# Kernel optimization log

Measured on AMD Instinct MI355X. Metric: run time of the kernel, lower is better.

## Reference

```python
import jax, jax.numpy as jnp
import numpy as np

B, S, D = 4, 2048, 1024
H = 16
HD = D // H  # head_dim = 64

def setup_inputs() -> dict:
    key = jax.random.key(0)
    kx, kq, ko = jax.random.split(key, 3)
    # xavier-uniform-like scale for weights
    lim_qkv = (6.0 / (D + 3 * D)) ** 0.5
    lim_o = (6.0 / (D + D)) ** 0.5
    return {
        "x": jax.random.normal(kx, (B, S, D), dtype=jnp.float32),
        "w_qkv": jax.random.uniform(kq, (3 * D, D), jnp.float32, -lim_qkv, lim_qkv),
        "b_qkv": jnp.zeros((3 * D,), jnp.float32),
        "w_o": jax.random.uniform(ko, (D, D), jnp.float32, -lim_o, lim_o),
        "b_o": jnp.zeros((D,), jnp.float32),
    }

def reference(x, w_qkv, b_qkv, w_o, b_o):
    b, s, _ = x.shape
    # QKV projection: torch Linear computes x @ W^T + b
    qkv = jnp.einsum("bsd,ed->bse", x, w_qkv) + b_qkv          # [B,S,3D]
    qkv = qkv.reshape(b, s, H, 3 * HD).transpose(0, 2, 1, 3)    # [B,H,S,3*hd]
    q, k, v = jnp.split(qkv, 3, axis=-1)                        # each [B,H,S,hd]
    scale = 1.0 / jnp.sqrt(jnp.asarray(HD, dtype=q.dtype))
    logits = jnp.einsum("bhqd,bhkd->bhqk", q, k) * scale        # [B,H,S,S]
    attn = jax.nn.softmax(logits, axis=-1)
    vals = jnp.einsum("bhqk,bhkd->bhqd", attn, v)               # [B,H,S,hd]
    vals = vals.transpose(0, 2, 1, 3).reshape(b, s, H * HD)     # [B,S,D]
    return jnp.einsum("bsd,ed->bse", vals, w_o) + b_o
```

## Files before the change

### kernel.cpp

```cpp
#include <hip/hip_runtime.h>
#include <hip/hip_bf16.h>


typedef __attribute__((ext_vector_type(4))) float f32x4;
typedef __attribute__((ext_vector_type(8))) short s16x8;
typedef __attribute__((ext_vector_type(2))) unsigned u32x2;
typedef __attribute__((ext_vector_type(4))) unsigned u32x4;

constexpr size_t PART_ELEMS = (size_t)8192 * 1024;

__device__ __forceinline__ unsigned short f2bf(float f) {
  __hip_bfloat16 h = __float2bfloat16(f);
  unsigned short u;
  __builtin_memcpy(&u, &h, 2);
  return u;
}
__device__ __forceinline__ unsigned pack2bf(float a, float b) {
  return (unsigned)f2bf(a) | ((unsigned)f2bf(b) << 16);
}
__device__ __forceinline__ float fexp2(float x) {
#if __has_builtin(__builtin_amdgcn_exp2f)
  return __builtin_amdgcn_exp2f(x);
#else
  float r; asm("v_exp_f32 %0, %1" : "=v"(r) : "v"(x)); return r;
#endif
}
__device__ __forceinline__ void gload_lds16(const void* g, void* l) {
  __builtin_amdgcn_global_load_lds(
      (const __attribute__((address_space(1))) unsigned*)g,
      (__attribute__((address_space(3))) unsigned*)l, 16, 0, 0);
}
__device__ __forceinline__ int swzs(int row, int col) {
  return row * 64 + (((col >> 3) ^ (row & 7)) << 3) + (col & 7);
}

__global__ __launch_bounds__(256) void cvt2_kernel(
    const float* __restrict__ a, unsigned short* __restrict__ oa,
    const float* __restrict__ b, unsigned short* __restrict__ ob) {
  const int bid = blockIdx.x;
  const float* in;
  unsigned short* out;
  size_t i;
  if (bid < 4096) {
    in = a; out = oa; i = ((size_t)bid * 256 + threadIdx.x) * 8;
  } else {
    in = b; out = ob; i = ((size_t)(bid - 4096) * 256 + threadIdx.x) * 8;
  }
  f32x4 v0 = *reinterpret_cast<const f32x4*>(in + i);
  f32x4 v1 = *reinterpret_cast<const f32x4*>(in + i + 4);
  u32x4 pk;
  pk.x = pack2bf(v0.x, v0.y); pk.y = pack2bf(v0.z, v0.w);
  pk.z = pack2bf(v1.x, v1.y); pk.w = pack2bf(v1.z, v1.w);
  *reinterpret_cast<u32x4*>(out + i) = pk;
}

__global__ __launch_bounds__(256) void cvt_kernel(const float* __restrict__ in,
                                                  unsigned short* __restrict__ out) {
  const size_t i = ((size_t)blockIdx.x * 256 + threadIdx.x) * 8;
  f32x4 v0 = *reinterpret_cast<const f32x4*>(in + i);
  f32x4 v1 = *reinterpret_cast<const f32x4*>(in + i + 4);
  u32x4 pk;
  pk.x = pack2bf(v0.x, v0.y); pk.y = pack2bf(v0.z, v0.w);
  pk.z = pack2bf(v1.x, v1.y); pk.w = pack2bf(v1.z, v1.w);
  *reinterpret_cast<u32x4*>(out + i) = pk;
}

template <bool SCATTER>
__global__ __launch_bounds__(256) void gemm_bb(
    const unsigned short* __restrict__ A, const unsigned short* __restrict__ Bw,
    const float* __restrict__ bias, void* __restrict__ Cptr,
    int M, int N, int K) {
  __shared__ short lds_a[128 * 32];
  __shared__ short lds_b[128 * 32];
  const int t = threadIdx.x;
  const int l = t & 63;
  const int w = t >> 6;
  const int id = blockIdx.x;
  const int xcd = id & 7;
  const int rr = id >> 3;
  const int bm = (xcd * 8 + (rr & 7)) * 128;
  const int bn = (rr >> 3) * 128;
  const int wr = (w >> 1) * 64;
  const int wc = (w & 1) * 64;
  const int lr = l & 15;
  const int lk = (l >> 4) * 8;

  f32x4 acc[4][4] = {};

  const int srow = w * 16 + (l >> 2);
  const int scol = (l & 3) * 8;
  short* adst0 = &lds_a[(w * 16) * 32];
  short* adst1 = &lds_a[(64 + w * 16) * 32];
  short* bdst0 = &lds_b[(w * 16) * 32];
  short* bdst1 = &lds_b[(64 + w * 16) * 32];

  for (int k0 = 0; k0 < K; k0 += 32) {
    const unsigned short* as = &A[(size_t)(bm + srow) * K + k0 + scol];
    gload_lds16(as, adst0);
    gload_lds16(as + (size_t)64 * K, adst1);
    const unsigned short* bs = &Bw[(size_t)(bn + srow) * K + k0 + scol];
    gload_lds16(bs, bdst0);
    gload_lds16(bs + (size_t)64 * K, bdst1);
    __syncthreads();

    s16x8 af[4], bfr[4];
#pragma unroll
    for (int mt = 0; mt < 4; ++mt)
      af[mt] = *reinterpret_cast<const s16x8*>(&lds_a[(wr + mt * 16 + lr) * 32 + lk]);
#pragma unroll
    for (int nt = 0; nt < 4; ++nt)
      bfr[nt] = *reinterpret_cast<const s16x8*>(&lds_b[(wc + nt * 16 + lr) * 32 + lk]);
#pragma unroll
    for (int mt = 0; mt < 4; ++mt)
#pragma unroll
      for (int nt = 0; nt < 4; ++nt)
        acc[mt][nt] = __builtin_amdgcn_mfma_f32_16x16x32_bf16(af[mt], bfr[nt], acc[mt][nt], 0, 0, 0);
    __syncthreads();
  }

#pragma unroll
  for (int mt = 0; mt < 4; ++mt) {
#pragma unroll
    for (int nt = 0; nt < 4; ++nt) {
#pragma unroll
      for (int r = 0; r < 4; ++r) {
        const int row = bm + wr + mt * 16 + (l >> 4) * 4 + r;
        const int col = bn + wc + nt * 16 + lr;
        const float vv = acc[mt][nt][r] + bias[col];
        if (SCATTER) {
          const int h = col / 192;
          const int rem = col - h * 192;
          const int part = rem >> 6;
          const int d = rem & 63;
          const int s = row & 2047;
          const size_t bh = (size_t)(row >> 11) * 16 + h;
          unsigned short* W = (unsigned short*)Cptr;
          float vvv = vv;
          if (part == 0) vvv *= 0.1803368801f;
          size_t off;
          if (part == 2)
            off = 2 * PART_ELEMS + (bh * 64 + d) * 2048 + s;
          else
            off = (size_t)part * PART_ELEMS + (bh * 2048 + s) * 64 + d;
          W[off] = f2bf(vvv);
        } else {
          ((float*)Cptr)[(size_t)row * N + col] = vv;
        }
      }
    }
  }
}

__global__ __launch_bounds__(512, 4) void attn_kernel(
    const unsigned short* __restrict__ ws, unsigned short* __restrict__ vals) {
  __shared__ short k_lds[2][64 * 64];
  __shared__ short vt_lds[2][64 * 64];
  __shared__ short p_lds[256 * 64];
  const int t = threadIdx.x;
  const int l = t & 63;
  const int w = t >> 6;
  const int lr = l & 15;
  const int lkh = l >> 4;
  const int f = blockIdx.x;
  const int xcd = f & 7;
  const int j = f >> 3;
  const int bh = xcd * 8 + (j & 7);
  const int qt = j >> 3;
  const int b = bh >> 4;
  const int h = bh & 15;
  const unsigned short* Qh  = ws + (size_t)bh * (2048 * 64);
  const unsigned short* Kh  = ws + PART_ELEMS + (size_t)bh * (2048 * 64);
  const unsigned short* VTh = ws + 2 * PART_ELEMS + (size_t)bh * (64 * 2048);

  const int srow = t >> 3;
  const int scol = (t & 7) * 8;

  s16x8 qf[2][2];
  {
    const unsigned short* qb = Qh + ((size_t)qt * 256 + w * 32 + lr) * 64 + lkh * 8;
    qf[0][0] = *reinterpret_cast<const s16x8*>(qb);
    qf[0][1] = *reinterpret_cast<const s16x8*>(qb + 32);
    qf[1][0] = *reinterpret_cast<const s16x8*>(qb + 16 * 64);
    qf[1][1] = *reinterpret_cast<const s16x8*>(qb + 16 * 64 + 32);
  }
  {
    s16x8 k0 = *reinterpret_cast<const s16x8*>(Kh + (size_t)srow * 64 + scol);
    s16x8 v0 = *reinterpret_cast<const s16x8*>(VTh + (size_t)srow * 2048 + scol);
    *reinterpret_cast<s16x8*>(&k_lds[0][swzs(srow, scol)])  = k0;
    *reinterpret_cast<s16x8*>(&vt_lds[0][swzs(srow, scol)]) = v0;
  }
  __syncthreads();

  f32x4 o_acc[2][4] = {};
  float l_s[2] = {0.f, 0.f};

  for (int kt = 0; kt < 32; ++kt) {
    const int cur = kt & 1;
    const int nxt = cur ^ 1;
    const bool pre = (kt + 1) < 32;

    s16x8 kr, vr;
    if (pre) {
      kr = *reinterpret_cast<const s16x8*>(Kh + ((size_t)(kt + 1) * 64 + srow) * 64 + scol);
      vr = *reinterpret_cast<const s16x8*>(VTh + (size_t)srow * 2048 + (kt + 1) * 64 + scol);
    }

    f32x4 s_acc[2][4] = {};
    {
      s16x8 kf[4][2];
#pragma unroll
      for (int nt = 0; nt < 4; ++nt) {
        kf[nt][0] = *reinterpret_cast<const s16x8*>(&k_lds[cur][swzs(nt * 16 + lr, lkh * 8)]);
        kf[nt][1] = *reinterpret_cast<const s16x8*>(&k_lds[cur][swzs(nt * 16 + lr, 32 + lkh * 8)]);
      }
      __builtin_amdgcn_s_setprio(1);
#pragma unroll
      for (int qh = 0; qh < 2; ++qh)
#pragma unroll
        for (int nt = 0; nt < 4; ++nt) {
          s_acc[qh][nt] = __builtin_amdgcn_mfma_f32_16x16x32_bf16(kf[nt][0], qf[qh][0], s_acc[qh][nt], 0, 0, 0);
          s_acc[qh][nt] = __builtin_amdgcn_mfma_f32_16x16x32_bf16(kf[nt][1], qf[qh][1], s_acc[qh][nt], 0, 0, 0);
        }
      __builtin_amdgcn_s_setprio(0);
    }

#pragma unroll
    for (int qh = 0; qh < 2; ++qh) {
      float rs = 0.f;
#pragma unroll
      for (int nt = 0; nt < 4; ++nt) {
        float p0 = fexp2(s_acc[qh][nt][0]);
        float p1 = fexp2(s_acc[qh][nt][1]);
        float p2 = fexp2(s_acc[qh][nt][2]);
        float p3 = fexp2(s_acc[qh][nt][3]);
        rs += (p0 + p1) + (p2 + p3);
        u32x2 pk;
        pk.x = pack2bf(p0, p1);
        pk.y = pack2bf(p2, p3);
        *reinterpret_cast<u32x2*>(&p_lds[swzs(w * 32 + qh * 16 + lr, nt * 16 + 4 * lkh)]) = pk;
      }
      l_s[qh] += rs;
    }

    {
      s16x8 vf[4][2];
#pragma unroll
      for (int nt = 0; nt < 4; ++nt) {
        vf[nt][0] = *reinterpret_cast<const s16x8*>(&vt_lds[cur][swzs(nt * 16 + lr, lkh * 8)]);
        vf[nt][1] = *reinterpret_cast<const s16x8*>(&vt_lds[cur][swzs(nt * 16 + lr, 32 + lkh * 8)]);
      }
      __builtin_amdgcn_s_setprio(1);
#pragma unroll
      for (int qh = 0; qh < 2; ++qh) {
        s16x8 pf0 = *reinterpret_cast<const s16x8*>(&p_lds[swzs(w * 32 + qh * 16 + lr, lkh * 8)]);
        s16x8 pf1 = *reinterpret_cast<const s16x8*>(&p_lds[swzs(w * 32 + qh * 16 + lr, 32 + lkh * 8)]);
#pragma unroll
        for (int nt = 0; nt < 4; ++nt) {
          o_acc[qh][nt] = __builtin_amdgcn_mfma_f32_16x16x32_bf16(pf0, vf[nt][0], o_acc[qh][nt], 0, 0, 0);
          o_acc[qh][nt] = __builtin_amdgcn_mfma_f32_16x16x32_bf16(pf1, vf[nt][1], o_acc[qh][nt], 0, 0, 0);
        }
      }
      __builtin_amdgcn_s_setprio(0);
    }

    if (pre) {
      *reinterpret_cast<s16x8*>(&k_lds[nxt][swzs(srow, scol)])  = kr;
      *reinterpret_cast<s16x8*>(&vt_lds[nxt][swzs(srow, scol)]) = vr;
    }
    __syncthreads();
  }

#pragma unroll
  for (int qh = 0; qh < 2; ++qh) {
    l_s[qh] += __shfl_xor(l_s[qh], 16);
    l_s[qh] += __shfl_xor(l_s[qh], 32);
  }
#pragma unroll
  for (int qh = 0; qh < 2; ++qh) {
#pragma unroll
    for (int r = 0; r < 4; ++r) {
      const float lv = __shfl(l_s[qh], 4 * lkh + r);
      const float inv = 1.0f / lv;
      const size_t row = (size_t)b * 2048 + qt * 256 + w * 32 + qh * 16 + lkh * 4 + r;
#pragma unroll
      for (int nt = 0; nt < 4; ++nt) {
        vals[row * 1024 + h * 64 + nt * 16 + lr] = f2bf(o_acc[qh][nt][r] * inv);
      }
    }
  }
}

extern "C" void kernel_launch(void* const* d_in, const int* in_sizes, int n_in,
                              void* d_out, int out_size, void* d_ws, size_t ws_size,
                              hipStream_t stream) {
  const float* x     = (const float*)d_in[0];
  const float* w_qkv = (const float*)d_in[1];
  const float* b_qkv = (const float*)d_in[2];
  const float* w_o   = (const float*)d_in[3];
  const float* b_o   = (const float*)d_in[4];
  float* out = (float*)d_out;

  unsigned short* xb     = (unsigned short*)d_ws;
  unsigned short* planes = xb + PART_ELEMS;
  unsigned short* wqkv_b = (unsigned short*)d_out;
  unsigned short* wo_b   = planes;

  cvt2_kernel<<<5632, 256, 0, stream>>>(x, xb, w_qkv, wqkv_b);
  gemm_bb<true><<<1536, 256, 0, stream>>>(
      xb, wqkv_b, b_qkv, planes, 8192, 3072, 1024);
  attn_kernel<<<512, 512, 0, stream>>>(planes, xb);
  cvt_kernel<<<512, 256, 0, stream>>>(w_o, wo_b);
  gemm_bb<false><<<512, 256, 0, stream>>>(
      xb, wo_b, b_o, out, 8192, 1024, 1024);
}
```

Baseline: 208.3 us.

## Use BK=64 GEMM tiles with XOR-swizzled LDS and hoist epilogue address math

The bf16 GEMM now stages a 64-wide K slice per iteration instead of 32, which halves the number of barrier pairs and loop trips over K. The LDS tiles use an XOR swizzle on 16-byte chunks so that fragment reads avoid bank conflicts. The scatter epilogue also computes head, part and base pointer once per column tile rather than per element. In exchange, LDS use per block doubles, which may reduce how many blocks fit on a CU.

```diff
diff --git a/kernel.cpp b/kernel.cpp
--- a/kernel.cpp
+++ b/kernel.cpp
@@ -70,8 +70,8 @@
     const unsigned short* __restrict__ A, const unsigned short* __restrict__ Bw,
     const float* __restrict__ bias, void* __restrict__ Cptr,
     int M, int N, int K) {
-  __shared__ short lds_a[128 * 32];
-  __shared__ short lds_b[128 * 32];
+  __shared__ short lds_a[128 * 64];
+  __shared__ short lds_b[128 * 64];
   const int t = threadIdx.x;
   const int l = t & 63;
   const int w = t >> 6;
@@ -83,68 +83,93 @@
   const int wr = (w >> 1) * 64;
   const int wc = (w & 1) * 64;
   const int lr = l & 15;
-  const int lk = (l >> 4) * 8;
+  const int lkh = l >> 4;
 
   f32x4 acc[4][4] = {};
 
-  const int srow = w * 16 + (l >> 2);
-  const int scol = (l & 3) * 8;
-  short* adst0 = &lds_a[(w * 16) * 32];
-  short* adst1 = &lds_a[(64 + w * 16) * 32];
-  short* bdst0 = &lds_b[(w * 16) * 32];
-  short* bdst1 = &lds_b[(64 + w * 16) * 32];
-
-  for (int k0 = 0; k0 < K; k0 += 32) {
-    const unsigned short* as = &A[(size_t)(bm + srow) * K + k0 + scol];
-    gload_lds16(as, adst0);
-    gload_lds16(as + (size_t)64 * K, adst1);
-    const unsigned short* bs = &Bw[(size_t)(bn + srow) * K + k0 + scol];
-    gload_lds16(bs, bdst0);
-    gload_lds16(bs + (size_t)64 * K, bdst1);
+  const int c8 = l >> 3;
+  const int gcol = ((l & 7) ^ c8) * 8;
+
+  for (int k0 = 0; k0 < K; k0 += 64) {
+    const unsigned short* as = &A[(size_t)(bm + w * 32 + c8) * K + k0 + gcol];
+    const unsigned short* bs = &Bw[(size_t)(bn + w * 32 + c8) * K + k0 + gcol];
+#pragma unroll
+    for (int c = 0; c < 4; ++c) {
+      gload_lds16(as + (size_t)(c * 8) * K, &lds_a[(w * 32 + c * 8) * 64]);
+      gload_lds16(bs + (size_t)(c * 8) * K, &lds_b[(w * 32 + c * 8) * 64]);
+    }
     __syncthreads();
 
-    s16x8 af[4], bfr[4];
-#pragma unroll
-    for (int mt = 0; mt < 4; ++mt)
-      af[mt] = *reinterpret_cast<const s16x8*>(&lds_a[(wr + mt * 16 + lr) * 32 + lk]);
-#pragma unroll
-    for (int nt = 0; nt < 4; ++nt)
-      bfr[nt] = *reinterpret_cast<const s16x8*>(&lds_b[(wc + nt * 16 + lr) * 32 + lk]);
-#pragma unroll
-    for (int mt = 0; mt < 4; ++mt)
-#pragma unroll
-      for (int nt = 0; nt < 4; ++nt)
-        acc[mt][nt] = __builtin_amdgcn_mfma_f32_16x16x32_bf16(af[mt], bfr[nt], acc[mt][nt], 0, 0, 0);
+#pragma unroll
+    for (int ki = 0; ki < 2; ++ki) {
+      s16x8 af[4], bfr[4];
+#pragma unroll
+      for (int mt = 0; mt < 4; ++mt) {
+        const int row = wr + mt * 16 + lr;
+        af[mt] = *reinterpret_cast<const s16x8*>(
+            &lds_a[row * 64 + ((((ki << 2) + lkh) ^ (lr & 7)) << 3)]);
+      }
+#pragma unroll
+      for (int nt = 0; nt < 4; ++nt) {
+        const int row = wc + nt * 16 + lr;
+        bfr[nt] = *reinterpret_cast<const s16x8*>(
+            &lds_b[row * 64 + ((((ki << 2) + lkh) ^ (lr & 7)) << 3)]);
+      }
+#pragma unroll
+      for (int mt = 0; mt < 4; ++mt)
+#pragma unroll
+        for (int nt = 0; nt < 4; ++nt)
+          acc[mt][nt] = __builtin_amdgcn_mfma_f32_16x16x32_bf16(af[mt], bfr[nt], acc[mt][nt], 0, 0, 0);
+    }
     __syncthreads();
   }
 
-#pragma unroll
-  for (int mt = 0; mt < 4; ++mt) {
+  if (SCATTER) {
+    unsigned short* W = (unsigned short*)Cptr;
+    const int s0 = (bm & 2047) + wr + (l >> 4) * 4;
+    const int batch = bm >> 11;
 #pragma unroll
     for (int nt = 0; nt < 4; ++nt) {
-#pragma unroll
-      for (int r = 0; r < 4; ++r) {
-        const int row = bm + wr + mt * 16 + (l >> 4) * 4 + r;
+      const int col = bn + wc + nt * 16 + lr;
+      const int h = col / 192;
+      const int rem = col - h * 192;
+      const int part = rem >> 6;
+      const int d = rem & 63;
+      const size_t bh = (size_t)batch * 16 + h;
+      const float bv = bias[col];
+      unsigned short* base;
+      int stride;
+      float scale;
+      if (part == 2) {
+        base = W + 2 * PART_ELEMS + (bh * 64 + d) * 2048;
+        stride = 1;
+        scale = 1.0f;
+      } else {
+        base = W + (size_t)part * PART_ELEMS + bh * 2048 * 64 + d;
+        stride = 64;
+        scale = (part == 0) ? 0.1803368801f : 1.0f;
+      }
+      unsigned short* p = base + (size_t)s0 * stride;
+#pragma unroll
+      for (int mt = 0; mt < 4; ++mt) {
+        unsigned short* pm = p + mt * 16 * stride;
+#pragma unroll
+        for (int r = 0; r < 4; ++r)
+          pm[r * stride] = f2bf((acc[mt][nt][r] + bv) * scale);
+      }
+    }
+  } else {
+    float* C = (float*)Cptr;
+#pragma unroll
+    for (int mt = 0; mt < 4; ++mt) {
+#pragma unroll
+      for (int nt = 0; nt < 4; ++nt) {
         const int col = bn + wc + nt * 16 + lr;
-        const float vv = acc[mt][nt][r] + bias[col];
-        if (SCATTER) {
-          const int h = col / 192;
-          const int rem = col - h * 192;
-          const int part = rem >> 6;
-          const int d = rem & 63;
-          const int s = row & 2047;
-          const size_t bh = (size_t)(row >> 11) * 16 + h;
-          unsigned short* W = (unsigned short*)Cptr;
-          float vvv = vv;
-          if (part == 0) vvv *= 0.1803368801f;
-          size_t off;
-          if (part == 2)
-            off = 2 * PART_ELEMS + (bh * 64 + d) * 2048 + s;
-          else
-            off = (size_t)part * PART_ELEMS + (bh * 2048 + s) * 64 + d;
-          W[off] = f2bf(vvv);
-        } else {
-          ((float*)Cptr)[(size_t)row * N + col] = vv;
+        const float bv = bias[col];
+#pragma unroll
+        for (int r = 0; r < 4; ++r) {
+          const int row = bm + wr + mt * 16 + (l >> 4) * 4 + r;
+          C[(size_t)row * N + col] = acc[mt][nt][r] + bv;
         }
       }
     }
```

New measurement: 193.7 us (median of 2 runs). 7.0% less time.
